# Kernel optimization log

Measured on AMD Instinct MI355X. Metric: run time of the kernel, lower is better.

The kernel has to match this reference:

```python
import jax, jax.numpy as jnp
import numpy as np

DIM = 64
NUM_HEADS = 8
HEAD_DIM = DIM // NUM_HEADS
INF = 1e9
EPS = 1e-10
S, R = 2048, 512  # n_seq (MSA rows), n_res


def setup_inputs() -> dict:
    key = jax.random.key(0)
    ks = jax.random.split(key, 8)
    m = jax.random.normal(ks[0], (S, R, DIM), dtype=jnp.float32)
    attn_mask = jnp.ones((S, R), dtype=jnp.float32)
    # weights stored as [in, out] (torch Linear applies x @ W.T; equivalent math)
    Wq = jax.random.normal(ks[1], (DIM, NUM_HEADS * HEAD_DIM), dtype=jnp.float32) * (DIM ** -0.5)
    Wk = jax.random.normal(ks[2], (DIM, HEAD_DIM), dtype=jnp.float32) * (DIM ** -0.5)
    Wv = jax.random.normal(ks[3], (DIM, HEAD_DIM), dtype=jnp.float32) * (DIM ** -0.5)
    Wg = jax.random.normal(ks[4], (DIM, NUM_HEADS * HEAD_DIM), dtype=jnp.float32) * (DIM ** -0.5)
    bg = jnp.ones((NUM_HEADS * HEAD_DIM,), dtype=jnp.float32)  # gating init: bias=1
    Wo = jax.random.normal(ks[5], (NUM_HEADS * HEAD_DIM, DIM), dtype=jnp.float32) * (DIM ** -0.5)
    bo = jnp.zeros((DIM,), dtype=jnp.float32)
    return {"m": m, "attn_mask": attn_mask, "Wq": Wq, "Wk": Wk, "Wv": Wv,
            "Wg": Wg, "bg": bg, "Wo": Wo, "bo": bo}


def reference(m, attn_mask, Wq, Wk, Wv, Wg, bg, Wo, bo):
    # masked mean-pool over residue axis -> per-row query  [S, dim]
    q = jnp.sum(m * attn_mask[..., None], axis=-2) / (jnp.sum(attn_mask, axis=-1)[..., None] + EPS)
    q = (q @ Wq).reshape(S, NUM_HEADS, HEAD_DIM) * (HEAD_DIM ** -0.5)  # [S, H, hd]
    k = m @ Wk  # [S, R, hd] (single shared K/V head)
    v = m @ Wv  # [S, R, hd]
    a = jnp.einsum('shc,src->shr', q, k)  # [S, H, R]
    a = a + (INF * (attn_mask - 1.0))[:, None, :]
    a = jax.nn.softmax(a, axis=-1)
    o = jnp.einsum('shr,src->shc', a, v)  # [S, H, hd]
    g = jax.nn.sigmoid(m @ Wg + bg).reshape(S, R, NUM_HEADS, HEAD_DIM)  # [S, R, H, hd]
    o = o[:, None, :, :] * g  # broadcast pooled output across residues
    o = o.reshape(S, R, NUM_HEADS * HEAD_DIM)
    return o @ Wo + bo  # [S, R, dim]
```

## Files before the change

### kernel.cpp

```cpp
#include <hip/hip_runtime.h>
#include <hip/hip_bf16.h>
#include <math.h>

#define NS 2048
#define NR 512
#define ND 64
#define NH 8
#define NSLOT 18
#define SPB 4

typedef __attribute__((ext_vector_type(4))) float f4;
typedef __attribute__((ext_vector_type(4))) unsigned u4;
typedef __attribute__((ext_vector_type(2))) unsigned u2;
typedef __attribute__((ext_vector_type(8))) short s8;

__device__ __forceinline__ short f2bf(float f) {
  unsigned u = __builtin_bit_cast(unsigned, f);
  u += 0x7fffu + ((u >> 16) & 1u);
  return (short)(u >> 16);
}
__device__ __forceinline__ unsigned cvtpk(float lo, float hi) {
  unsigned r;
  asm("v_cvt_pk_bf16_f32 %0, %1, %2" : "=v"(r) : "v"(lo), "v"(hi));
  return r;
}
__device__ __forceinline__ float bflo(unsigned u) { return __builtin_bit_cast(float, u << 16); }
__device__ __forceinline__ float bfhi(unsigned u) { return __builtin_bit_cast(float, u & 0xffff0000u); }

__device__ __forceinline__ int swz(int r, int c) {
  return ((r << 7) + (c << 1)) ^ ((r & 7) << 4);
}
__device__ __forceinline__ int kvaddr(int r, int c) {
  return ((r << 5) + (c << 1)) ^ ((r & 4) << 2);
}

__global__ void prep_kernel(const float* __restrict__ Wk, const float* __restrict__ Wv,
                            const float* __restrict__ Wg, const float* __restrict__ Wo,
                            short* __restrict__ ws) {
  for (int i = threadIdx.x; i < NSLOT * 64; i += blockDim.x) {
    const int slot = i >> 6, lane = i & 63;
    const int col = lane & 15, kq = (lane >> 4) * 8;
    s8 f;
    if (slot < 2) {
      #pragma unroll
      for (int jj = 0; jj < 8; ++jj) {
        const int k = slot * 32 + kq + jj;
        f[jj] = f2bf(col < 8 ? Wk[k * 8 + col] : Wv[k * 8 + col - 8]);
      }
    } else if (slot < 10) {
      const int idx = slot - 2, ks = idx >> 2, nt = idx & 3;
      #pragma unroll
      for (int jj = 0; jj < 8; ++jj) {
        const int k = ks * 32 + kq + jj;
        f[jj] = f2bf(Wg[k * 64 + 4 * col + nt]);
      }
    } else {
      const int idx = slot - 10, ks = idx >> 2, nt = idx & 3;
      #pragma unroll
      for (int jj = 0; jj < 8; ++jj) {
        const int k = ks * 32 + kq + jj;
        f[jj] = f2bf(Wo[k * 64 + 4 * col + nt]);
      }
    }
    *reinterpret_cast<s8*>(ws + (size_t)i * 8) = f;
  }
}

__global__ __launch_bounds__(512, 4)
void ga_kernel(const float* __restrict__ gm, const float* __restrict__ gmask,
               const float* __restrict__ Wq, const float* __restrict__ bgp,
               const float* __restrict__ bop, const short* __restrict__ ws,
               float* __restrict__ gout)
{
  __shared__ short fragB[NSLOT * 64 * 8];
  __shared__ unsigned short kvb_s[NR * 16];
  __shared__ short tmpb[8][16 * ND];
  __shared__ float maskb[SPB][NR];
  __shared__ float red[8][ND];
  __shared__ float ofl[ND];
  __shared__ float bgo[2][ND];

  const int t    = threadIdx.x;
  const int lane = t & 63;
  const int wv   = t >> 6;
  const int arow = lane & 15;
  const int g    = lane >> 4;
  const int kq   = g * 8;
  const int s0   = blockIdx.x * SPB;

  const f4 zf = {0, 0, 0, 0};

  for (int i = t; i < NSLOT * 64; i += 512)
    *reinterpret_cast<s8*>(&fragB[i * 8]) = *reinterpret_cast<const s8*>(ws + (size_t)i * 8);
  for (int i = t; i < SPB * NR; i += 512)
    (&maskb[0][0])[i] = gmask[(size_t)s0 * NR + i];
  if (t < 64)       bgo[0][t]      = bgp[t];
  else if (t < 128) bgo[1][t - 64] = bop[t - 64];
  __syncthreads();

  f4 pl0, pl1, pl2, pl3;

  auto a_finish = [&](int mt, int jn, f4 a0, f4 a1, f4 b0, f4 b1) {
    const int row = wv * 64 + mt * 16 + arow;
    const float mk = maskb[jn][row];
    pl0 += a0 * mk; pl1 += a1 * mk; pl2 += b0 * mk; pl3 += b1 * mk;
    u4 ua, ub;
    ua[0] = cvtpk(a0.x, a0.y); ua[1] = cvtpk(a0.z, a0.w);
    ua[2] = cvtpk(a1.x, a1.y); ua[3] = cvtpk(a1.z, a1.w);
    ub[0] = cvtpk(b0.x, b0.y); ub[1] = cvtpk(b0.z, b0.w);
    ub[2] = cvtpk(b1.x, b1.y); ub[3] = cvtpk(b1.z, b1.w);
    const s8 mA = __builtin_bit_cast(s8, ua);
    const s8 mB = __builtin_bit_cast(s8, ub);
    const s8 kf0 = *reinterpret_cast<const s8*>(&fragB[(0 * 64 + lane) * 8]);
    const s8 kf1 = *reinterpret_cast<const s8*>(&fragB[(1 * 64 + lane) * 8]);
    f4 acc = zf;
    acc = __builtin_amdgcn_mfma_f32_16x16x32_bf16(mA, kf0, acc, 0, 0, 0);
    acc = __builtin_amdgcn_mfma_f32_16x16x32_bf16(mB, kf1, acc, 0, 0, 0);
    char* kvb = reinterpret_cast<char*>(&kvb_s[0]);
    const int r0 = wv * 64 + mt * 16;
    #pragma unroll
    for (int q = 0; q < 4; ++q)
      *reinterpret_cast<unsigned short*>(kvb + kvaddr(r0 + g * 4 + q, arow)) =
          (unsigned short)f2bf(acc[q]);
  };

  auto a_end = [&]() {
    #pragma unroll
    for (int off = 8; off >= 1; off >>= 1) {
      pl0.x += __shfl_xor(pl0.x, off); pl0.y += __shfl_xor(pl0.y, off);
      pl0.z += __shfl_xor(pl0.z, off); pl0.w += __shfl_xor(pl0.w, off);
      pl1.x += __shfl_xor(pl1.x, off); pl1.y += __shfl_xor(pl1.y, off);
      pl1.z += __shfl_xor(pl1.z, off); pl1.w += __shfl_xor(pl1.w, off);
      pl2.x += __shfl_xor(pl2.x, off); pl2.y += __shfl_xor(pl2.y, off);
      pl2.z += __shfl_xor(pl2.z, off); pl2.w += __shfl_xor(pl2.w, off);
      pl3.x += __shfl_xor(pl3.x, off); pl3.y += __shfl_xor(pl3.y, off);
      pl3.z += __shfl_xor(pl3.z, off); pl3.w += __shfl_xor(pl3.w, off);
    }
    if (arow == 0) {
      *reinterpret_cast<f4*>(&red[wv][kq])          = pl0;
      *reinterpret_cast<f4*>(&red[wv][kq + 4])      = pl1;
      *reinterpret_cast<f4*>(&red[wv][32 + kq])     = pl2;
      *reinterpret_cast<f4*>(&red[wv][32 + kq + 4]) = pl3;
    }
  };

  auto attn = [&](int j) {
    float qv_l = 0.f;
    #pragma unroll
    for (int w = 0; w < 8; ++w) qv_l += red[w][lane];
    float dn = 0.f;
    #pragma unroll
    for (int i = 0; i < 8; ++i) dn += maskb[j][lane + 64 * i];
    #pragma unroll
    for (int off = 32; off; off >>= 1) dn += __shfl_xor(dn, off);
    const f4 w0 = *reinterpret_cast<const f4*>(Wq + lane * 64 + wv * 8);
    const f4 w1 = *reinterpret_cast<const f4*>(Wq + lane * 64 + wv * 8 + 4);
    float a0 = qv_l * w0.x, a1 = qv_l * w0.y, a2 = qv_l * w0.z, a3 = qv_l * w0.w;
    float a4 = qv_l * w1.x, a5 = qv_l * w1.y, a6 = qv_l * w1.z, a7 = qv_l * w1.w;
    #pragma unroll
    for (int off = 32; off; off >>= 1) {
      a0 += __shfl_xor(a0, off); a1 += __shfl_xor(a1, off);
      a2 += __shfl_xor(a2, off); a3 += __shfl_xor(a3, off);
      a4 += __shfl_xor(a4, off); a5 += __shfl_xor(a5, off);
      a6 += __shfl_xor(a6, off); a7 += __shfl_xor(a7, off);
    }
    const float qs = 0.35355339059327373f / (dn + 1e-10f);
    const float q0 = a0 * qs, q1 = a1 * qs, q2 = a2 * qs, q3 = a3 * qs;
    const float q4 = a4 * qs, q5 = a5 * qs, q6 = a6 * qs, q7 = a7 * qs;

    const char* kvb = reinterpret_cast<const char*>(&kvb_s[0]);
    float lg[8];
    float mx = -3.4e38f;
    #pragma unroll
    for (int i = 0; i < 8; ++i) {
      const int r = lane + 64 * i;
      const u4 kk = *reinterpret_cast<const u4*>(kvb + ((r << 5) ^ ((r & 4) << 2)));
      float acc = q0 * bflo(kk[0]) + q1 * bfhi(kk[0])
                + q2 * bflo(kk[1]) + q3 * bfhi(kk[1])
                + q4 * bflo(kk[2]) + q5 * bfhi(kk[2])
                + q6 * bflo(kk[3]) + q7 * bfhi(kk[3]);
      lg[i] = acc + 1e9f * (maskb[j][r] - 1.0f);
      mx = fmaxf(mx, lg[i]);
    }
    #pragma unroll
    for (int off = 32; off; off >>= 1) mx = fmaxf(mx, __shfl_xor(mx, off));
    float sum = 0.f;
    #pragma unroll
    for (int i = 0; i < 8; ++i) { lg[i] = __expf(lg[i] - mx); sum += lg[i]; }
    #pragma unroll
    for (int off = 32; off; off >>= 1) sum += __shfl_xor(sum, off);
    const float inv = 1.0f / sum;
    float po[8] = {0, 0, 0, 0, 0, 0, 0, 0};
    #pragma unroll
    for (int i = 0; i < 8; ++i) {
      const int r = lane + 64 * i;
      const float a = lg[i] * inv;
      const u4 vvv = *reinterpret_cast<const u4*>(kvb + (((r << 5) + 16) ^ ((r & 4) << 2)));
      po[0] += a * bflo(vvv[0]); po[1] += a * bfhi(vvv[0]);
      po[2] += a * bflo(vvv[1]); po[3] += a * bfhi(vvv[1]);
      po[4] += a * bflo(vvv[2]); po[5] += a * bfhi(vvv[2]);
      po[6] += a * bflo(vvv[3]); po[7] += a * bfhi(vvv[3]);
    }
    #pragma unroll
    for (int off = 32; off; off >>= 1) {
      #pragma unroll
      for (int c = 0; c < 8; ++c) po[c] += __shfl_xor(po[c], off);
    }
    #pragma unroll
    for (int c = 0; c < 8; ++c) if (lane == c) ofl[wv * 8 + c] = po[c];
  };

  auto b_iter = [&](int mt, const float* mrowB, float* orow) {
    const int r0 = wv * 64 + mt * 16;
    const float* p = mrowB + (r0 + arow) * ND + kq;
    const f4 a0 = *reinterpret_cast<const f4*>(p);
    const f4 a1 = *reinterpret_cast<const f4*>(p + 4);
    const f4 b0 = *reinterpret_cast<const f4*>(p + 32);
    const f4 b1 = *reinterpret_cast<const f4*>(p + 36);
    u4 ua, ub;
    ua[0] = cvtpk(a0.x, a0.y); ua[1] = cvtpk(a0.z, a0.w);
    ua[2] = cvtpk(a1.x, a1.y); ua[3] = cvtpk(a1.z, a1.w);
    ub[0] = cvtpk(b0.x, b0.y); ub[1] = cvtpk(b0.z, b0.w);
    ub[2] = cvtpk(b1.x, b1.y); ub[3] = cvtpk(b1.z, b1.w);
    const s8 mA = __builtin_bit_cast(s8, ua);
    const s8 mB = __builtin_bit_cast(s8, ub);

    f4 accG[4] = {zf, zf, zf, zf};
    #pragma unroll
    for (int nt = 0; nt < 4; ++nt) {
      const s8 wg0 = *reinterpret_cast<const s8*>(&fragB[((2 + nt) * 64 + lane) * 8]);
      const s8 wg1 = *reinterpret_cast<const s8*>(&fragB[((6 + nt) * 64 + lane) * 8]);
      accG[nt] = __builtin_amdgcn_mfma_f32_16x16x32_bf16(mA, wg0, accG[nt], 0, 0, 0);
      accG[nt] = __builtin_amdgcn_mfma_f32_16x16x32_bf16(mB, wg1, accG[nt], 0, 0, 0);
    }

    const f4 ofv = *reinterpret_cast<const f4*>(&ofl[4 * arow]);
    const f4 bgv = *reinterpret_cast<const f4*>(&bgo[0][4 * arow]);
    short* tmpw = &tmpb[wv][0];
    #pragma unroll
    for (int q2 = 0; q2 < 4; ++q2) {
      float v[4];
      #pragma unroll
      for (int nt = 0; nt < 4; ++nt)
        v[nt] = ofv[nt] / (1.0f + __expf(-(accG[nt][q2] + bgv[nt])));
      u2 w;
      w[0] = cvtpk(v[0], v[1]);
      w[1] = cvtpk(v[2], v[3]);
      *reinterpret_cast<u2*>(reinterpret_cast<char*>(tmpw) + swz(g * 4 + q2, 4 * arow)) = w;
    }
    asm volatile("s_waitcnt lgkmcnt(0)" ::: "memory");
    __builtin_amdgcn_sched_barrier(0);

    f4 accO[4] = {zf, zf, zf, zf};
    #pragma unroll
    for (int ks = 0; ks < 2; ++ks) {
      const s8 aF = *reinterpret_cast<const s8*>(
          reinterpret_cast<const char*>(tmpw) + swz(arow, ks * 32 + kq));
      #pragma unroll
      for (int nt = 0; nt < 4; ++nt) {
        const s8 woF = *reinterpret_cast<const s8*>(&fragB[((10 + ks * 4 + nt) * 64 + lane) * 8]);
        accO[nt] = __builtin_amdgcn_mfma_f32_16x16x32_bf16(aF, woF, accO[nt], 0, 0, 0);
      }
    }
    const f4 bov = *reinterpret_cast<const f4*>(&bgo[1][4 * arow]);
    #pragma unroll
    for (int q2 = 0; q2 < 4; ++q2) {
      f4 ov;
      ov.x = accO[0][q2] + bov.x;
      ov.y = accO[1][q2] + bov.y;
      ov.z = accO[2][q2] + bov.z;
      ov.w = accO[3][q2] + bov.w;
      *reinterpret_cast<f4*>(orow + (r0 + g * 4 + q2) * ND + 4 * arow) = ov;
    }
  };

  pl0 = pl1 = pl2 = pl3 = zf;
  {
    const float* mA_ = gm + (size_t)s0 * NR * ND;
    #pragma unroll 1
    for (int mt = 0; mt < 4; ++mt) {
      const float* p = mA_ + (wv * 64 + mt * 16 + arow) * ND + kq;
      const f4 a0 = *reinterpret_cast<const f4*>(p);
      const f4 a1 = *reinterpret_cast<const f4*>(p + 4);
      const f4 b0 = *reinterpret_cast<const f4*>(p + 32);
      const f4 b1 = *reinterpret_cast<const f4*>(p + 36);
      a_finish(mt, 0, a0, a1, b0, b1);
    }
    a_end();
  }
  __syncthreads();

  #pragma unroll 1
  for (int j = 0; j < SPB; ++j) {
    attn(j);
    __syncthreads();

    const float* mB_ = gm + (size_t)(s0 + j) * NR * ND;
    float* oB_ = gout + (size_t)(s0 + j) * NR * ND;

    if (j < SPB - 1) {
      pl0 = pl1 = pl2 = pl3 = zf;
      const float* mA_ = gm + (size_t)(s0 + j + 1) * NR * ND;
      #pragma unroll 1
      for (int mt = 0; mt < 4; ++mt) {
        const float* pa = mA_ + (wv * 64 + mt * 16 + arow) * ND + kq;
        const f4 a0 = *reinterpret_cast<const f4*>(pa);
        const f4 a1 = *reinterpret_cast<const f4*>(pa + 4);
        const f4 b0 = *reinterpret_cast<const f4*>(pa + 32);
        const f4 b1 = *reinterpret_cast<const f4*>(pa + 36);
        b_iter(mt, mB_, oB_);
        a_finish(mt, j + 1, a0, a1, b0, b1);
      }
      a_end();
    } else {
      #pragma unroll 1
      for (int mt = 0; mt < 4; ++mt) b_iter(mt, mB_, oB_);
    }
    __syncthreads();
  }
}

extern "C" void kernel_launch(void* const* d_in, const int* in_sizes, int n_in,
                              void* d_out, int out_size, void* d_ws, size_t ws_size,
                              hipStream_t stream) {
  const float* m    = (const float*)d_in[0];
  const float* mask = (const float*)d_in[1];
  const float* Wq   = (const float*)d_in[2];
  const float* Wk   = (const float*)d_in[3];
  const float* Wv   = (const float*)d_in[4];
  const float* Wg   = (const float*)d_in[5];
  const float* bg   = (const float*)d_in[6];
  const float* Wo   = (const float*)d_in[7];
  const float* bo   = (const float*)d_in[8];
  float* out = (float*)d_out;
  short* ws  = (short*)d_ws;

  prep_kernel<<<dim3(1), dim3(512), 0, stream>>>(Wk, Wv, Wg, Wo, ws);
  ga_kernel<<<dim3(NS / SPB), dim3(512), 0, stream>>>(m, mask, Wq, bg, bo, ws, out);
}
```

Measured before the change: 164.8 us.

## Split fused kernel into separate attention and gating kernels over row halves

Replaces the single software-pipelined kernel with two kernels: one computes pooled attention output per MSA row into a workspace buffer, the other applies gating and output projection. Work is split into two halves, and the gate kernel walks rows in reverse order, intending to reuse m still resident in cache. This removes the in-block cross-row pipelining and the large shared fragment buffer, which should improve occupancy. The cost is a second pass over m that may miss cache, plus extra launches.

```diff
diff --git a/kernel.cpp b/kernel.cpp
--- a/kernel.cpp
+++ b/kernel.cpp
@@ -7,7 +7,8 @@
 #define ND 64
 #define NH 8
 #define NSLOT 18
-#define SPB 4
+#define NSH (NS/2)
+#define O_OFF 32768
 
 typedef __attribute__((ext_vector_type(4))) float f4;
 typedef __attribute__((ext_vector_type(4))) unsigned u4;
@@ -67,18 +68,13 @@
 }
 
 __global__ __launch_bounds__(512, 4)
-void ga_kernel(const float* __restrict__ gm, const float* __restrict__ gmask,
-               const float* __restrict__ Wq, const float* __restrict__ bgp,
-               const float* __restrict__ bop, const short* __restrict__ ws,
-               float* __restrict__ gout)
+void k1_attn(const float* __restrict__ gm, const float* __restrict__ gmask,
+             const float* __restrict__ Wq, const short* __restrict__ ws,
+             float* __restrict__ o_out, int s_base)
 {
-  __shared__ short fragB[NSLOT * 64 * 8];
   __shared__ unsigned short kvb_s[NR * 16];
-  __shared__ short tmpb[8][16 * ND];
-  __shared__ float maskb[SPB][NR];
+  __shared__ float maskb[NR];
   __shared__ float red[8][ND];
-  __shared__ float ofl[ND];
-  __shared__ float bgo[2][ND];
 
   const int t    = threadIdx.x;
   const int lane = t & 63;
@@ -86,23 +82,26 @@
   const int arow = lane & 15;
   const int g    = lane >> 4;
   const int kq   = g * 8;
-  const int s0   = blockIdx.x * SPB;
+  const int s    = s_base + blockIdx.x;
 
   const f4 zf = {0, 0, 0, 0};
-
-  for (int i = t; i < NSLOT * 64; i += 512)
-    *reinterpret_cast<s8*>(&fragB[i * 8]) = *reinterpret_cast<const s8*>(ws + (size_t)i * 8);
-  for (int i = t; i < SPB * NR; i += 512)
-    (&maskb[0][0])[i] = gmask[(size_t)s0 * NR + i];
-  if (t < 64)       bgo[0][t]      = bgp[t];
-  else if (t < 128) bgo[1][t - 64] = bop[t - 64];
+  const float* mrow = gm + (size_t)s * NR * ND;
+
+  for (int i = t; i < NR; i += 512) maskb[i] = gmask[(size_t)s * NR + i];
+  const s8 kf0 = *reinterpret_cast<const s8*>(ws + (size_t)(0 * 64 + lane) * 8);
+  const s8 kf1 = *reinterpret_cast<const s8*>(ws + (size_t)(1 * 64 + lane) * 8);
   __syncthreads();
 
-  f4 pl0, pl1, pl2, pl3;
-
-  auto a_finish = [&](int mt, int jn, f4 a0, f4 a1, f4 b0, f4 b1) {
+  f4 pl0 = zf, pl1 = zf, pl2 = zf, pl3 = zf;
+  #pragma unroll
+  for (int mt = 0; mt < 4; ++mt) {
     const int row = wv * 64 + mt * 16 + arow;
-    const float mk = maskb[jn][row];
+    const float mk = maskb[row];
+    const float* p = mrow + row * ND + kq;
+    const f4 a0 = *reinterpret_cast<const f4*>(p);
+    const f4 a1 = *reinterpret_cast<const f4*>(p + 4);
+    const f4 b0 = *reinterpret_cast<const f4*>(p + 32);
+    const f4 b1 = *reinterpret_cast<const f4*>(p + 36);
     pl0 += a0 * mk; pl1 += a1 * mk; pl2 += b0 * mk; pl3 += b1 * mk;
     u4 ua, ub;
     ua[0] = cvtpk(a0.x, a0.y); ua[1] = cvtpk(a0.z, a0.w);
@@ -111,8 +110,6 @@
     ub[2] = cvtpk(b1.x, b1.y); ub[3] = cvtpk(b1.z, b1.w);
     const s8 mA = __builtin_bit_cast(s8, ua);
     const s8 mB = __builtin_bit_cast(s8, ub);
-    const s8 kf0 = *reinterpret_cast<const s8*>(&fragB[(0 * 64 + lane) * 8]);
-    const s8 kf1 = *reinterpret_cast<const s8*>(&fragB[(1 * 64 + lane) * 8]);
     f4 acc = zf;
     acc = __builtin_amdgcn_mfma_f32_16x16x32_bf16(mA, kf0, acc, 0, 0, 0);
     acc = __builtin_amdgcn_mfma_f32_16x16x32_bf16(mB, kf1, acc, 0, 0, 0);
@@ -122,35 +119,33 @@
     for (int q = 0; q < 4; ++q)
       *reinterpret_cast<unsigned short*>(kvb + kvaddr(r0 + g * 4 + q, arow)) =
           (unsigned short)f2bf(acc[q]);
-  };
-
-  auto a_end = [&]() {
-    #pragma unroll
-    for (int off = 8; off >= 1; off >>= 1) {
-      pl0.x += __shfl_xor(pl0.x, off); pl0.y += __shfl_xor(pl0.y, off);
-      pl0.z += __shfl_xor(pl0.z, off); pl0.w += __shfl_xor(pl0.w, off);
-      pl1.x += __shfl_xor(pl1.x, off); pl1.y += __shfl_xor(pl1.y, off);
-      pl1.z += __shfl_xor(pl1.z, off); pl1.w += __shfl_xor(pl1.w, off);
-      pl2.x += __shfl_xor(pl2.x, off); pl2.y += __shfl_xor(pl2.y, off);
-      pl2.z += __shfl_xor(pl2.z, off); pl2.w += __shfl_xor(pl2.w, off);
-      pl3.x += __shfl_xor(pl3.x, off); pl3.y += __shfl_xor(pl3.y, off);
-      pl3.z += __shfl_xor(pl3.z, off); pl3.w += __shfl_xor(pl3.w, off);
-    }
-    if (arow == 0) {
-      *reinterpret_cast<f4*>(&red[wv][kq])          = pl0;
-      *reinterpret_cast<f4*>(&red[wv][kq + 4])      = pl1;
-      *reinterpret_cast<f4*>(&red[wv][32 + kq])     = pl2;
-      *reinterpret_cast<f4*>(&red[wv][32 + kq + 4]) = pl3;
-    }
-  };
-
-  auto attn = [&](int j) {
+  }
+  #pragma unroll
+  for (int off = 8; off >= 1; off >>= 1) {
+    pl0.x += __shfl_xor(pl0.x, off); pl0.y += __shfl_xor(pl0.y, off);
+    pl0.z += __shfl_xor(pl0.z, off); pl0.w += __shfl_xor(pl0.w, off);
+    pl1.x += __shfl_xor(pl1.x, off); pl1.y += __shfl_xor(pl1.y, off);
+    pl1.z += __shfl_xor(pl1.z, off); pl1.w += __shfl_xor(pl1.w, off);
+    pl2.x += __shfl_xor(pl2.x, off); pl2.y += __shfl_xor(pl2.y, off);
+    pl2.z += __shfl_xor(pl2.z, off); pl2.w += __shfl_xor(pl2.w, off);
+    pl3.x += __shfl_xor(pl3.x, off); pl3.y += __shfl_xor(pl3.y, off);
+    pl3.z += __shfl_xor(pl3.z, off); pl3.w += __shfl_xor(pl3.w, off);
+  }
+  if (arow == 0) {
+    *reinterpret_cast<f4*>(&red[wv][kq])          = pl0;
+    *reinterpret_cast<f4*>(&red[wv][kq + 4])      = pl1;
+    *reinterpret_cast<f4*>(&red[wv][32 + kq])     = pl2;
+    *reinterpret_cast<f4*>(&red[wv][32 + kq + 4]) = pl3;
+  }
+  __syncthreads();
+
+  {
     float qv_l = 0.f;
     #pragma unroll
     for (int w = 0; w < 8; ++w) qv_l += red[w][lane];
     float dn = 0.f;
     #pragma unroll
-    for (int i = 0; i < 8; ++i) dn += maskb[j][lane + 64 * i];
+    for (int i = 0; i < 8; ++i) dn += maskb[lane + 64 * i];
     #pragma unroll
     for (int off = 32; off; off >>= 1) dn += __shfl_xor(dn, off);
     const f4 w0 = *reinterpret_cast<const f4*>(Wq + lane * 64 + wv * 8);
@@ -179,7 +174,7 @@
                 + q2 * bflo(kk[1]) + q3 * bfhi(kk[1])
                 + q4 * bflo(kk[2]) + q5 * bfhi(kk[2])
                 + q6 * bflo(kk[3]) + q7 * bfhi(kk[3]);
-      lg[i] = acc + 1e9f * (maskb[j][r] - 1.0f);
+      lg[i] = acc + 1e9f * (maskb[r] - 1.0f);
       mx = fmaxf(mx, lg[i]);
     }
     #pragma unroll
@@ -207,12 +202,50 @@
       for (int c = 0; c < 8; ++c) po[c] += __shfl_xor(po[c], off);
     }
     #pragma unroll
-    for (int c = 0; c < 8; ++c) if (lane == c) ofl[wv * 8 + c] = po[c];
-  };
-
-  auto b_iter = [&](int mt, const float* mrowB, float* orow) {
+    for (int c = 0; c < 8; ++c)
+      if (lane == c) o_out[(size_t)s * ND + wv * 8 + c] = po[c];
+  }
+}
+
+__global__ __launch_bounds__(512, 4)
+void k3_gate(const float* __restrict__ gm, const float* __restrict__ bgp,
+             const float* __restrict__ bop, const short* __restrict__ ws,
+             const float* __restrict__ o_in, float* __restrict__ gout, int s_base)
+{
+  __shared__ short fragW[16 * 64 * 8];
+  __shared__ short tmpb[8][16 * ND];
+  __shared__ float ofl[ND];
+  __shared__ float bgo[2][ND];
+
+  const int t    = threadIdx.x;
+  const int lane = t & 63;
+  const int wv   = t >> 6;
+  const int arow = lane & 15;
+  const int g    = lane >> 4;
+  const int kq   = g * 8;
+  const int s    = s_base + (NSH - 1 - (int)blockIdx.x);
+
+  const f4 zf = {0, 0, 0, 0};
+  const float* mrow = gm + (size_t)s * NR * ND;
+  float* orow = gout + (size_t)s * NR * ND;
+
+  for (int i = t; i < 16 * 64; i += 512)
+    *reinterpret_cast<s8*>(&fragW[i * 8]) =
+        *reinterpret_cast<const s8*>(ws + (size_t)(2 * 64 + i) * 8);
+  if (t < 64)       bgo[0][t]      = bgp[t];
+  else if (t < 128) bgo[1][t - 64] = bop[t - 64];
+  if (t >= 128 && t < 192) ofl[t - 128] = o_in[(size_t)s * ND + (t - 128)];
+  __syncthreads();
+
+  const f4 ofv = *reinterpret_cast<const f4*>(&ofl[4 * arow]);
+  const f4 bgv = *reinterpret_cast<const f4*>(&bgo[0][4 * arow]);
+  const f4 bov = *reinterpret_cast<const f4*>(&bgo[1][4 * arow]);
+  short* tmpw = &tmpb[wv][0];
+
+  #pragma unroll
+  for (int mt = 0; mt < 4; ++mt) {
     const int r0 = wv * 64 + mt * 16;
-    const float* p = mrowB + (r0 + arow) * ND + kq;
+    const float* p = mrow + (r0 + arow) * ND + kq;
     const f4 a0 = *reinterpret_cast<const f4*>(p);
     const f4 a1 = *reinterpret_cast<const f4*>(p + 4);
     const f4 b0 = *reinterpret_cast<const f4*>(p + 32);
@@ -228,15 +261,12 @@
     f4 accG[4] = {zf, zf, zf, zf};
     #pragma unroll
     for (int nt = 0; nt < 4; ++nt) {
-      const s8 wg0 = *reinterpret_cast<const s8*>(&fragB[((2 + nt) * 64 + lane) * 8]);
-      const s8 wg1 = *reinterpret_cast<const s8*>(&fragB[((6 + nt) * 64 + lane) * 8]);
+      const s8 wg0 = *reinterpret_cast<const s8*>(&fragW[((0 + nt) * 64 + lane) * 8]);
+      const s8 wg1 = *reinterpret_cast<const s8*>(&fragW[((4 + nt) * 64 + lane) * 8]);
       accG[nt] = __builtin_amdgcn_mfma_f32_16x16x32_bf16(mA, wg0, accG[nt], 0, 0, 0);
       accG[nt] = __builtin_amdgcn_mfma_f32_16x16x32_bf16(mB, wg1, accG[nt], 0, 0, 0);
     }
 
-    const f4 ofv = *reinterpret_cast<const f4*>(&ofl[4 * arow]);
-    const f4 bgv = *reinterpret_cast<const f4*>(&bgo[0][4 * arow]);
-    short* tmpw = &tmpb[wv][0];
     #pragma unroll
     for (int q2 = 0; q2 < 4; ++q2) {
       float v[4];
@@ -258,11 +288,10 @@
           reinterpret_cast<const char*>(tmpw) + swz(arow, ks * 32 + kq));
       #pragma unroll
       for (int nt = 0; nt < 4; ++nt) {
-        const s8 woF = *reinterpret_cast<const s8*>(&fragB[((10 + ks * 4 + nt) * 64 + lane) * 8]);
+        const s8 woF = *reinterpret_cast<const s8*>(&fragW[((8 + ks * 4 + nt) * 64 + lane) * 8]);
         accO[nt] = __builtin_amdgcn_mfma_f32_16x16x32_bf16(aF, woF, accO[nt], 0, 0, 0);
       }
     }
-    const f4 bov = *reinterpret_cast<const f4*>(&bgo[1][4 * arow]);
     #pragma unroll
     for (int q2 = 0; q2 < 4; ++q2) {
       f4 ov;
@@ -272,51 +301,6 @@
       ov.w = accO[3][q2] + bov.w;
       *reinterpret_cast<f4*>(orow + (r0 + g * 4 + q2) * ND + 4 * arow) = ov;
     }
-  };
-
-  pl0 = pl1 = pl2 = pl3 = zf;
-  {
-    const float* mA_ = gm + (size_t)s0 * NR * ND;
-    #pragma unroll 1
-    for (int mt = 0; mt < 4; ++mt) {
-      const float* p = mA_ + (wv * 64 + mt * 16 + arow) * ND + kq;
-      const f4 a0 = *reinterpret_cast<const f4*>(p);
-      const f4 a1 = *reinterpret_cast<const f4*>(p + 4);
-      const f4 b0 = *reinterpret_cast<const f4*>(p + 32);
-      const f4 b1 = *reinterpret_cast<const f4*>(p + 36);
-      a_finish(mt, 0, a0, a1, b0, b1);
-    }
-    a_end();
-  }
-  __syncthreads();
-
-  #pragma unroll 1
-  for (int j = 0; j < SPB; ++j) {
-    attn(j);
-    __syncthreads();
-
-    const float* mB_ = gm + (size_t)(s0 + j) * NR * ND;
-    float* oB_ = gout + (size_t)(s0 + j) * NR * ND;
-
-    if (j < SPB - 1) {
-      pl0 = pl1 = pl2 = pl3 = zf;
-      const float* mA_ = gm + (size_t)(s0 + j + 1) * NR * ND;
-      #pragma unroll 1
-      for (int mt = 0; mt < 4; ++mt) {
-        const float* pa = mA_ + (wv * 64 + mt * 16 + arow) * ND + kq;
-        const f4 a0 = *reinterpret_cast<const f4*>(pa);
-        const f4 a1 = *reinterpret_cast<const f4*>(pa + 4);
-        const f4 b0 = *reinterpret_cast<const f4*>(pa + 32);
-        const f4 b1 = *reinterpret_cast<const f4*>(pa + 36);
-        b_iter(mt, mB_, oB_);
-        a_finish(mt, j + 1, a0, a1, b0, b1);
-      }
-      a_end();
-    } else {
-      #pragma unroll 1
-      for (int mt = 0; mt < 4; ++mt) b_iter(mt, mB_, oB_);
-    }
-    __syncthreads();
   }
 }
 
@@ -334,7 +318,11 @@
   const float* bo   = (const float*)d_in[8];
   float* out = (float*)d_out;
   short* ws  = (short*)d_ws;
+  float* o_buf = (float*)((char*)d_ws + O_OFF);
 
   prep_kernel<<<dim3(1), dim3(512), 0, stream>>>(Wk, Wv, Wg, Wo, ws);
-  ga_kernel<<<dim3(NS / SPB), dim3(512), 0, stream>>>(m, mask, Wq, bg, bo, ws, out);
-}
+  k1_attn<<<dim3(NSH), dim3(512), 0, stream>>>(m, mask, Wq, ws, o_buf, 0);
+  k3_gate<<<dim3(NSH), dim3(512), 0, stream>>>(m, bg, bo, ws, o_buf, out, 0);
+  k1_attn<<<dim3(NSH), dim3(512), 0, stream>>>(m, mask, Wq, ws, o_buf, NSH);
+  k3_gate<<<dim3(NSH), dim3(512), 0, stream>>>(m, bg, bo, ws, o_buf, out, NSH);
+}
```

Measured after the change: 190.6 us. +15.6%, slower.
